# Optimization experiments

Measured on AMD Instinct MI355X. Metric: run time of the kernel, lower is better.

## Reference

```python
import jax, jax.numpy as jnp
import numpy as np

# Constants describing the (equal-length) ragged batch and CRF tag space
B, L = 64, 512                 # 64 sequences of 512 segment-tokens each
C = 1024                       # fuse_embedding_channel
NUM_CLASSES = 5                # real field classes
NUM_TAGS = NUM_CLASSES + 2     # + START + STOP
START, STOP = NUM_CLASSES, NUM_CLASSES + 1
NEG = -10000.0


def setup_inputs() -> dict:
    key = jax.random.key(0)
    k1, k2, k3, k4 = jax.random.split(key, 4)
    fuse_embeddings = jax.random.normal(k1, (B * L, C), jnp.float32)
    label_class = jax.random.randint(k2, (B * L,), 0, NUM_CLASSES)
    # classification head params (Linear C -> NUM_TAGS)
    W = jax.random.normal(k3, (NUM_TAGS, C), jnp.float32) * 0.02
    b = jnp.zeros((NUM_TAGS,), jnp.float32)
    # CRF transition matrix: transitions[next, prev]
    transitions = jax.random.normal(k4, (NUM_TAGS, NUM_TAGS), jnp.float32) * 0.01
    transitions = transitions.at[START, :].set(NEG).at[:, STOP].set(NEG)
    return {"fuse_embeddings": fuse_embeddings, "label_class": label_class,
            "W": W, "b": b, "transitions": transitions}


def _crf_nll_sum(feats, tags, transitions):
    """Sum over batch of (forward_alg score - gold score).
    feats: [B, L, T] emissions, tags: [B, L] int, transitions: [T, T] (next, prev)."""
    # --- forward algorithm (batched log-sum-exp recurrence) ---
    init = jnp.full((B, NUM_TAGS), NEG, feats.dtype).at[:, START].set(0.0)

    def step(fv, emit):
        # fv: [B, prev], emit: [B, next]
        fv_new = jax.nn.logsumexp(fv[:, None, :] + transitions[None, :, :], axis=2) + emit
        return fv_new, None

    fv, _ = jax.lax.scan(step, init, jnp.swapaxes(feats, 0, 1))  # scan over L
    fwd_score = jax.nn.logsumexp(fv + transitions[STOP][None, :], axis=1)  # [B]

    # --- gold sentence score ---
    tags_ext = jnp.concatenate([jnp.full((B, 1), START, tags.dtype), tags], axis=1)
    emit_sc = jnp.take_along_axis(feats, tags[..., None], axis=2)[..., 0].sum(axis=1)
    trans_sc = transitions[tags_ext[:, 1:], tags_ext[:, :-1]].sum(axis=1)
    gold = emit_sc + trans_sc + transitions[STOP, tags[:, -1]]
    return (fwd_score - gold).sum()


def reference(fuse_embeddings, label_class, W, b, transitions):
    # per-token linear projection to tag logits
    pred_class = fuse_embeddings @ W.T + b          # [N, NUM_TAGS]
    feats = pred_class.reshape(B, L, NUM_TAGS)
    tags = label_class.reshape(B, L)
    score = _crf_nll_sum(feats, tags, transitions)
    return (jnp.reshape(score, (1,)), label_class.astype(jnp.int32), pred_class)
```

## Files before the change

kernel.cpp:

```cpp
#include <hip/hip_runtime.h>

#define BSEQ 64
#define LSEQ 512
#define CCH  1024
#define NT   7
#define NC   5
#define NTOK (BSEQ*LSEQ)
#define START_TAG 5
#define STOP_TAG  6
#define NEGV (-10000.0f)
#define GRID_LOGITS 1024

typedef float vfloat4 __attribute__((ext_vector_type(4)));

template<int CTRL, int RMASK, int BMASK>
__device__ __forceinline__ float dpp_add(float x) {
    int y = __builtin_amdgcn_update_dpp(0, __float_as_int(x), CTRL, RMASK, BMASK, true);
    return x + __int_as_float(y);
}
__device__ __forceinline__ float wave_sum(float x) {
    x = dpp_add<0x111, 0xF, 0xF>(x);
    x = dpp_add<0x112, 0xF, 0xF>(x);
    x = dpp_add<0x114, 0xF, 0xF>(x);
    x = dpp_add<0x118, 0xF, 0xF>(x);
    x = dpp_add<0x142, 0xA, 0xF>(x);
    x = dpp_add<0x143, 0xC, 0xF>(x);
    return x;
}

__device__ __forceinline__ float lse5(const float v0, const float v1, const float v2,
                                      const float v3, const float v4) {
    float m = fmaxf(fmaxf(fmaxf(v0, v1), fmaxf(v2, v3)), v4);
    float s = __expf(v0 - m) + __expf(v1 - m) + __expf(v2 - m)
            + __expf(v3 - m) + __expf(v4 - m);
    return m + __logf(s);
}

__global__ __launch_bounds__(256)
void k_logits(const float* __restrict__ X, const float* __restrict__ W,
              const float* __restrict__ bvec, const int* __restrict__ lab,
              float* __restrict__ out)
{
    __shared__ float Wl[NT][CCH];
    __shared__ float bl[NT];

    const int lane = threadIdx.x & 63;
    const int wid  = (blockIdx.x * 256 + threadIdx.x) >> 6;
    const int nw   = (GRID_LOGITS * 256) >> 6;

    vfloat4 xb[3][4];

    #define ISSUE_PHASE(p, slot)                                                   \
        if ((p) < 8) {                                                             \
            const int G_ = (p) >> 2, k_ = (p) & 3;                                 \
            _Pragma("unroll")                                                      \
            for (int j = 0; j < 4; j++) {                                          \
                const size_t row_ = (size_t)(wid + (G_*4 + j) * nw);               \
                const vfloat4* xp_ = (const vfloat4*)(X + row_ * CCH) + (k_*64 + lane); \
                xb[slot][j] = __builtin_nontemporal_load(xp_);                     \
            }                                                                      \
        }

    ISSUE_PHASE(0, 0)
    ISSUE_PHASE(1, 1)

    {
        const vfloat4* W4  = (const vfloat4*)W;
        vfloat4*       Wl4 = (vfloat4*)(&Wl[0][0]);
        for (int i = threadIdx.x; i < NT*CCH/4; i += 256) Wl4[i] = W4[i];
        if (threadIdx.x < NT) bl[threadIdx.x] = bvec[threadIdx.x];
    }
    __syncthreads();

    float* outP = out + 1 + NTOK;

    float acc[4][NT];
    #pragma unroll
    for (int j = 0; j < 4; j++)
        #pragma unroll
        for (int t = 0; t < NT; t++) acc[j][t] = 0.0f;

    #pragma unroll
    for (int p = 0; p < 8; ++p) {
        const int slot = p % 3;
        const int k    = p & 3;

        ISSUE_PHASE(p + 2, (p + 2) % 3)

        vfloat4 wreg[NT];
        {
            const int cb = (k*64 + lane) * 4;
            #pragma unroll
            for (int t = 0; t < NT; t++)
                wreg[t] = *(const vfloat4*)(&Wl[t][cb]);
        }

        #pragma unroll
        for (int j = 0; j < 4; j++) {
            #pragma unroll
            for (int t = 0; t < NT; t++) {
                acc[j][t] = fmaf(xb[slot][j].x, wreg[t].x,
                            fmaf(xb[slot][j].y, wreg[t].y,
                            fmaf(xb[slot][j].z, wreg[t].z,
                            fmaf(xb[slot][j].w, wreg[t].w, acc[j][t]))));
            }
        }

        if (k == 3) {
            const int G = p >> 2;
            #pragma unroll
            for (int j = 0; j < 4; j++) {
                const size_t row = (size_t)(wid + (G*4 + j) * nw);
                #pragma unroll
                for (int t = 0; t < NT; t++) {
                    float s = wave_sum(acc[j][t]);
                    if (lane == 63) outP[row * NT + t] = s + bl[t];
                    acc[j][t] = 0.0f;
                }
            }
        }
    }
    #undef ISSUE_PHASE

    for (int i = blockIdx.x * 256 + threadIdx.x; i < NTOK; i += GRID_LOGITS * 256)
        out[1 + i] = (float)lab[i];
    if (blockIdx.x == 0 && threadIdx.x == 0) out[0] = 0.0f;
}

__global__ __launch_bounds__(320)
void k_crf(const float* __restrict__ dout_ro, const int* __restrict__ lab,
           const float* __restrict__ trans, float* __restrict__ score)
{
    __shared__ float E[LSEQ*NT];
    __shared__ float M2[32*25];
    __shared__ float T[49];
    __shared__ float u_sh[NC];
    __shared__ float gred[5];

    const int b   = blockIdx.x;
    const int tid = threadIdx.x;
    const float* feats = dout_ro + 1 + NTOK + (size_t)b * (LSEQ*NT);

    for (int i = tid; i < LSEQ*NT; i += 320) E[i] = feats[i];
    if (tid < 49) T[tid] = trans[tid];
    __syncthreads();

    if (tid < NC) u_sh[tid] = T[tid*NT + START_TAG] + E[tid];

    float g = 0.0f;
    for (int l = tid; l < LSEQ; l += 320) {
        const int t  = lab[b*LSEQ + l];
        const int tp = (l == 0) ? START_TAG : lab[b*LSEQ + l - 1];
        g += E[l*NT + t] + T[t*NT + tp];
    }
    if (tid == 0) g += T[STOP_TAG*NT + lab[b*LSEQ + LSEQ - 1]];
    {
        float gs = wave_sum(g);
        if ((tid & 63) == 63) gred[tid >> 6] = gs;
    }

    float TR[NC*NC];
    #pragma unroll
    for (int j = 0; j < NC; j++)
        #pragma unroll
        for (int k = 0; k < NC; k++) TR[j*NC + k] = T[j*NT + k];

    const int chunk = tid / NC;
    const int basis = tid - chunk * NC;
    float fv[NC];
    #pragma unroll
    for (int j = 0; j < NC; j++) fv[j] = (j == basis) ? 0.0f : NEGV;

    const int l0    = (chunk == 0) ? 1 : chunk * 8;
    const int steps = (chunk == 0) ? 7 : 8;
    for (int s = 0; s < steps; s++) {
        const int l = l0 + s;
        float fn[NC];
        #pragma unroll
        for (int j = 0; j < NC; j++) {
            fn[j] = lse5(fv[0] + TR[j*NC+0], fv[1] + TR[j*NC+1], fv[2] + TR[j*NC+2],
                         fv[3] + TR[j*NC+3], fv[4] + TR[j*NC+4]) + E[l*NT + j];
        }
        #pragma unroll
        for (int j = 0; j < NC; j++) fv[j] = fn[j];
    }
    __syncthreads();
    #pragma unroll
    for (int j = 0; j < NC; j++) E[chunk*25 + basis*NC + j] = fv[j];

    int n = 64, cur = 0;
    while (n > 1) {
        __syncthreads();
        const float* in = (cur == 0) ? (const float*)E : (const float*)M2;
        float*       ob = (cur == 0) ? M2 : E;
        const int half = n >> 1;
        for (int e2 = tid; e2 < half*25; e2 += 320) {
            const int p = e2 / 25, r = e2 - p*25;
            const int i = r / NC, j = r - (r/NC)*NC;
            const float* A  = in + (2*p)*25 + i*NC;
            const float* Bm = in + (2*p + 1)*25 + j;
            ob[p*25 + r] = lse5(A[0] + Bm[0], A[1] + Bm[NC], A[2] + Bm[2*NC],
                                A[3] + Bm[3*NC], A[4] + Bm[4*NC]);
        }
        cur ^= 1; n = half;
    }
    __syncthreads();

    if (tid == 0) {
        float gg = gred[0] + gred[1] + gred[2] + gred[3] + gred[4];
        const float* M = (cur == 0) ? (const float*)E : (const float*)M2;
        float v[NC];
        #pragma unroll
        for (int j = 0; j < NC; j++)
            v[j] = lse5(u_sh[0] + M[0*NC+j], u_sh[1] + M[1*NC+j], u_sh[2] + M[2*NC+j],
                        u_sh[3] + M[3*NC+j], u_sh[4] + M[4*NC+j]);
        float fwd = lse5(v[0] + T[STOP_TAG*NT+0], v[1] + T[STOP_TAG*NT+1],
                         v[2] + T[STOP_TAG*NT+2], v[3] + T[STOP_TAG*NT+3],
                         v[4] + T[STOP_TAG*NT+4]);
        atomicAdd(score, fwd - gg);
    }
}

extern "C" void kernel_launch(void* const* d_in, const int* in_sizes, int n_in,
                              void* d_out, int out_size, void* d_ws, size_t ws_size,
                              hipStream_t stream) {
    const float* X     = (const float*)d_in[0];
    const int*   lab   = (const int*)  d_in[1];
    const float* W     = (const float*)d_in[2];
    const float* bvec  = (const float*)d_in[3];
    const float* trans = (const float*)d_in[4];
    float* out = (float*)d_out;

    k_logits<<<GRID_LOGITS, 256, 0, stream>>>(X, W, bvec, lab, out);
    k_crf<<<BSEQ, 320, 0, stream>>>(out, lab, trans, out);
}
```

Baseline: 214.0 us.

## Fuse logits and CRF into one cooperative kernel with grid sync

Replaces the two-kernel pipeline with a single cooperative kernel. Each block computes logits for 32 contiguous tokens, keeps their emissions in LDS, and builds a local 5x5 log-semiring transfer matrix plus a partial gold score. After a grid-wide sync, 64 blocks chain 16 partial matrices each to finish the forward score. This removes the second kernel launch and the re-read of emissions from global memory, at the cost of a grid barrier and a token-to-block mapping that changes the memory access pattern.

```diff
diff --git a/kernel.cpp b/kernel.cpp
--- a/kernel.cpp
+++ b/kernel.cpp
@@ -1,4 +1,7 @@
 #include <hip/hip_runtime.h>
+#include <hip/hip_cooperative_groups.h>
+
+namespace cg = cooperative_groups;
 
 #define BSEQ 64
 #define LSEQ 512
@@ -10,6 +13,13 @@
 #define STOP_TAG  6
 #define NEGV (-10000.0f)
 #define GRID_LOGITS 1024
+#define FGRID 1024
+#define FBLK  256
+
+#define WS_M   0
+#define WS_G   32768
+#define WS_U   33792
+#define WS_TOT 34304
 
 typedef float vfloat4 __attribute__((ext_vector_type(4)));
 
@@ -34,6 +44,204 @@
     float s = __expf(v0 - m) + __expf(v1 - m) + __expf(v2 - m)
             + __expf(v3 - m) + __expf(v4 - m);
     return m + __logf(s);
+}
+
+__global__ __launch_bounds__(256)
+void k_fused(const float* __restrict__ X, const float* __restrict__ W,
+             const float* __restrict__ bvec, const int* __restrict__ lab,
+             const float* __restrict__ trans, float* __restrict__ out,
+             float* __restrict__ ws)
+{
+    __shared__ float Wl[NT][CCH];
+    __shared__ float bl[NT];
+    __shared__ float Tl[49];
+    __shared__ float E_lds[32][5];
+    __shared__ float Msub[4*25];
+    __shared__ float Cb[2*25];
+    __shared__ float Mbuf[16*25];
+
+    const int tid  = threadIdx.x;
+    const int lane = tid & 63;
+    const int wv   = tid >> 6;
+    const int bx   = blockIdx.x;
+
+    if (bx == 0 && tid == 0) atomicExch(out, 0.0f);
+
+    vfloat4 xb[3][4];
+    const size_t rbase = (size_t)bx * 32 + wv;
+
+    #define ISSUE_PHASE(p, slot)                                                    \
+        if ((p) < 8) {                                                              \
+            const int G_ = (p) >> 2, k_ = (p) & 3;                                  \
+            _Pragma("unroll")                                                       \
+            for (int j = 0; j < 4; j++) {                                           \
+                const size_t row_ = rbase + (size_t)((G_*4 + j) * 4);               \
+                const vfloat4* xp_ = (const vfloat4*)(X + row_ * CCH) + (k_*64 + lane); \
+                xb[slot][j] = __builtin_nontemporal_load(xp_);                      \
+            }                                                                       \
+        }
+
+    ISSUE_PHASE(0, 0)
+    ISSUE_PHASE(1, 1)
+
+    {
+        const vfloat4* W4  = (const vfloat4*)W;
+        vfloat4*       Wl4 = (vfloat4*)(&Wl[0][0]);
+        for (int i = tid; i < NT*CCH/4; i += FBLK) Wl4[i] = W4[i];
+        if (tid < NT) bl[tid] = bvec[tid];
+        if (tid < 49) Tl[tid] = trans[tid];
+        const int gidx = bx * FBLK + tid;
+        if (gidx < NTOK) out[1 + gidx] = (float)lab[gidx];
+    }
+    __syncthreads();
+
+    float* outP = out + 1 + NTOK;
+
+    float acc[4][NT];
+    #pragma unroll
+    for (int j = 0; j < 4; j++)
+        #pragma unroll
+        for (int t = 0; t < NT; t++) acc[j][t] = 0.0f;
+
+    #pragma unroll
+    for (int p = 0; p < 8; ++p) {
+        const int slot = p % 3;
+        const int k    = p & 3;
+
+        ISSUE_PHASE(p + 2, (p + 2) % 3)
+
+        vfloat4 wreg[NT];
+        {
+            const int cb = (k*64 + lane) * 4;
+            #pragma unroll
+            for (int t = 0; t < NT; t++)
+                wreg[t] = *(const vfloat4*)(&Wl[t][cb]);
+        }
+
+        #pragma unroll
+        for (int j = 0; j < 4; j++) {
+            #pragma unroll
+            for (int t = 0; t < NT; t++) {
+                acc[j][t] = fmaf(xb[slot][j].x, wreg[t].x,
+                            fmaf(xb[slot][j].y, wreg[t].y,
+                            fmaf(xb[slot][j].z, wreg[t].z,
+                            fmaf(xb[slot][j].w, wreg[t].w, acc[j][t]))));
+            }
+        }
+
+        if (k == 3) {
+            const int G = p >> 2;
+            #pragma unroll
+            for (int j = 0; j < 4; j++) {
+                const int m = G*4 + j;
+                const size_t row = rbase + (size_t)(m * 4);
+                const int rloc = wv + m*4;
+                #pragma unroll
+                for (int t = 0; t < NT; t++) {
+                    float s = wave_sum(acc[j][t]);
+                    if (lane == 63) {
+                        const float e = s + bl[t];
+                        outP[row * NT + t] = e;
+                        if (t < NC) E_lds[rloc][t] = e;
+                    }
+                    acc[j][t] = 0.0f;
+                }
+            }
+        }
+    }
+    #undef ISSUE_PHASE
+
+    __syncthreads();
+
+    const int sub = bx & 15;
+    const int bat = bx >> 4;
+
+    if (wv == 0) {
+        if (lane < 20) {
+            const int sc = lane / 5, basis = lane - sc*5;
+            float TR[25];
+            #pragma unroll
+            for (int j = 0; j < NC; j++)
+                #pragma unroll
+                for (int k = 0; k < NC; k++) TR[j*5+k] = Tl[j*7+k];
+            float fv[5];
+            #pragma unroll
+            for (int j = 0; j < NC; j++) fv[j] = (j == basis) ? 0.0f : NEGV;
+            const int s0 = (sub == 0 && sc == 0) ? 1 : sc*8;
+            const int s1 = sc*8 + 8;
+            for (int s = s0; s < s1; ++s) {
+                float fn[5];
+                #pragma unroll
+                for (int j = 0; j < NC; j++)
+                    fn[j] = lse5(fv[0]+TR[j*5+0], fv[1]+TR[j*5+1], fv[2]+TR[j*5+2],
+                                 fv[3]+TR[j*5+3], fv[4]+TR[j*5+4]) + E_lds[s][j];
+                #pragma unroll
+                for (int j = 0; j < NC; j++) fv[j] = fn[j];
+            }
+            #pragma unroll
+            for (int j = 0; j < NC; j++) Msub[sc*25 + basis*5 + j] = fv[j];
+        }
+        if (lane < 50) {
+            const int pp = lane / 25, r = lane - pp*25, i = r/5, jj = r - (r/5)*5;
+            const float* A = &Msub[(2*pp)*25 + i*5];
+            const float* B = &Msub[(2*pp+1)*25 + jj];
+            Cb[pp*25 + r] = lse5(A[0]+B[0], A[1]+B[5], A[2]+B[10], A[3]+B[15], A[4]+B[20]);
+        }
+        if (lane < 25) {
+            const int i = lane/5, jj = lane - i*5;
+            const float* A = &Cb[i*5];
+            const float* B = &Cb[25 + jj];
+            ws[WS_M + (size_t)bx*32 + lane] =
+                lse5(A[0]+B[0], A[1]+B[5], A[2]+B[10], A[3]+B[15], A[4]+B[20]);
+        }
+    } else if (wv == 1) {
+        float g = 0.0f;
+        if (lane < 32) {
+            const int lg = bx*32 + lane;
+            const int t  = lab[lg];
+            const int tp = ((lg & (LSEQ-1)) == 0) ? START_TAG : lab[lg - 1];
+            g = E_lds[lane][t] + Tl[t*7 + tp];
+        }
+        float gs = wave_sum(g);
+        if (lane == 63) ws[WS_G + bx] = gs;
+    } else if (wv == 2) {
+        if (sub == 0 && lane < NC)
+            ws[WS_U + bat*8 + lane] = Tl[lane*7 + START_TAG] + E_lds[0][lane];
+    }
+
+    __threadfence();
+    cg::this_grid().sync();
+
+    if (bx < BSEQ && wv == 0) {
+        if (lane < 25) {
+            #pragma unroll
+            for (int m = 0; m < 16; ++m)
+                Mbuf[m*25 + lane] = ws[WS_M + ((size_t)bx*16 + m)*32 + lane];
+        }
+        float gp = (lane < 16) ? ws[WS_G + bx*16 + lane] : 0.0f;
+        float gtot = wave_sum(gp);
+        gtot = __shfl(gtot, 63);
+        if (lane < NC) {
+            const int j = lane;
+            float fvr = ws[WS_U + bx*8 + j];
+            for (int m = 0; m < 16; ++m) {
+                const float f0 = __shfl(fvr, 0), f1 = __shfl(fvr, 1), f2 = __shfl(fvr, 2),
+                            f3 = __shfl(fvr, 3), f4 = __shfl(fvr, 4);
+                const float* M = &Mbuf[m*25];
+                fvr = lse5(f0 + M[0*5+j], f1 + M[1*5+j], f2 + M[2*5+j],
+                           f3 + M[3*5+j], f4 + M[4*5+j]);
+            }
+            const float v0 = __shfl(fvr, 0), v1 = __shfl(fvr, 1), v2 = __shfl(fvr, 2),
+                        v3 = __shfl(fvr, 3), v4 = __shfl(fvr, 4);
+            if (j == 0) {
+                float fwd = lse5(v0 + Tl[STOP_TAG*7+0], v1 + Tl[STOP_TAG*7+1],
+                                 v2 + Tl[STOP_TAG*7+2], v3 + Tl[STOP_TAG*7+3],
+                                 v4 + Tl[STOP_TAG*7+4]);
+                float gold = gtot + Tl[STOP_TAG*7 + lab[bx*LSEQ + LSEQ - 1]];
+                atomicAdd(out, fwd - gold);
+            }
+        }
+    }
 }
 
 __global__ __launch_bounds__(256)
@@ -230,6 +438,19 @@
     const float* bvec  = (const float*)d_in[3];
     const float* trans = (const float*)d_in[4];
     float* out = (float*)d_out;
+    float* wsf = (float*)d_ws;
+
+    int maxB = 0;
+    hipError_t oe = hipOccupancyMaxActiveBlocksPerMultiprocessor(&maxB, k_fused, FBLK, 0);
+    if (oe == hipSuccess && maxB >= 4 && wsf != nullptr &&
+        ws_size >= (size_t)WS_TOT * sizeof(float)) {
+        void* kargs[] = {(void*)&X, (void*)&W, (void*)&bvec, (void*)&lab,
+                         (void*)&trans, (void*)&out, (void*)&wsf};
+        hipError_t le = hipLaunchCooperativeKernel((const void*)k_fused,
+                                                   dim3(FGRID), dim3(FBLK),
+                                                   kargs, 0, stream);
+        if (le == hipSuccess) return;
+    }
 
     k_logits<<<GRID_LOGITS, 256, 0, stream>>>(X, W, bvec, lab, out);
     k_crf<<<BSEQ, 320, 0, stream>>>(out, lab, trans, out);
```

Measured after the change: 211.7 us. No clear change (-1.1%).
